# Kernel optimization log

Hardware: AMD Instinct MI355X
Metric: run time of the kernel (lower is better)

## Reference

```python
import jax, jax.numpy as jnp
import numpy as np

NB_HEAD = 8
SIZE_PER_HEAD = 64
EMB = 512  # word embedding dim; output_dim = NB_HEAD*SIZE_PER_HEAD = 512
B, S = 8, 4096


def setup_inputs() -> dict:
    key = jax.random.key(0)
    ks = jax.random.split(key, 8)
    return {
        "Q_seq": jax.random.normal(ks[0], (B, S, EMB), dtype=jnp.float32),
        "K_seq": jax.random.normal(ks[1], (B, S, EMB), dtype=jnp.float32),
        "V_seq": jax.random.normal(ks[2], (B, S, EMB), dtype=jnp.float32),
        "Q_len": jax.random.randint(ks[3], (B, 1), 0, S, dtype=jnp.int32),
        "V_len": jax.random.randint(ks[4], (B, 1), 0, SIZE_PER_HEAD, dtype=jnp.int32),
        "WQ": jax.random.normal(ks[5], (EMB, NB_HEAD * SIZE_PER_HEAD), dtype=jnp.float32),
        "WK": jax.random.normal(ks[6], (EMB, NB_HEAD * SIZE_PER_HEAD), dtype=jnp.float32),
        "WV": jax.random.normal(ks[7], (EMB, NB_HEAD * SIZE_PER_HEAD), dtype=jnp.float32),
    }


def _proj_heads(x, W):
    # [B,S,E] @ [E,H*d] -> [B,H,S,d]
    y = jnp.einsum('bse,eo->bso', x, W)
    y = y.reshape(y.shape[0], y.shape[1], NB_HEAD, SIZE_PER_HEAD)
    return jnp.transpose(y, (0, 2, 1, 3))


def reference(Q_seq, K_seq, V_seq, Q_len, V_len, WQ, WK, WV):
    H, d = NB_HEAD, SIZE_PER_HEAD
    Q = _proj_heads(Q_seq, WQ)  # [B,H,S,d]
    K = _proj_heads(K_seq, WK)
    V = _proj_heads(V_seq, WV)

    A = (Q * K) / jnp.asarray(d, Q.dtype) ** 0.5  # elementwise, [B,H,S,d]

    # TF code transposes A to [B,d,S,H] and masks along axis 1 (size d) using
    # V_len, then transposes back. Equivalent: additive mask on the LAST axis.
    vmask = jax.nn.one_hot(V_len[:, 0], d, dtype=A.dtype)       # [B,d]
    vmask = 1.0 - jnp.cumsum(vmask, axis=1)                      # [B,d]
    A = A - (1.0 - vmask)[:, None, None, :] * 1e12

    A = jax.nn.softmax(A, axis=-1)  # softmax over d (last axis), as tf.nn.softmax

    O = A * V                              # [B,H,S,d]
    O = jnp.transpose(O, (0, 2, 1, 3))     # [B,S,H,d]
    O = O.reshape(O.shape[0], O.shape[1], H * d)  # [B,S,H*d]

    # multiplicative mask over sequence axis using Q_len
    qmask = jax.nn.one_hot(Q_len[:, 0], O.shape[1], dtype=O.dtype)  # [B,S]
    qmask = 1.0 - jnp.cumsum(qmask, axis=1)
    return O * qmask[:, :, None]
```

## Files before the change

kernel.cpp:

```cpp
#include <hip/hip_runtime.h>

typedef unsigned short u16;
typedef _Float16 f16;
typedef _Float16 f16x4 __attribute__((ext_vector_type(4)));
typedef _Float16 f16x8 __attribute__((ext_vector_type(8)));
typedef float    f32x4 __attribute__((ext_vector_type(4)));

#define BATCH 8
#define SEQ   4096
#define EMB   512
#define NCOL  512

__global__ __launch_bounds__(256) void prep_w(
    const float* __restrict__ Wq, const float* __restrict__ Wk,
    const float* __restrict__ Wv, u16* __restrict__ out)
{
  __shared__ u16 tile[64][65];
  const int z = blockIdx.z;
  const float* in = (z < 2) ? Wq : (z < 4) ? Wk : Wv;
  const bool lo = (z == 1 || z == 3);
  u16* o = out + (size_t)z * EMB * NCOL;
  const int r0 = blockIdx.y * 64, c0 = blockIdx.x * 64;
  const int tx = threadIdx.x, ty = threadIdx.y;
#pragma unroll
  for (int i = 0; i < 16; ++i) {
    const int r = ty * 16 + i;
    const float x = in[(size_t)(r0 + r) * NCOL + (c0 + tx)];
    const f16 h = (f16)x;
    const f16 v = lo ? (f16)((x - (float)h) * 256.0f) : h;
    tile[r][tx] = __builtin_bit_cast(u16, v);
  }
  __syncthreads();
#pragma unroll
  for (int i = 0; i < 16; ++i) {
    const int rr = ty * 16 + i;
    o[(size_t)(c0 + rr) * EMB + (r0 + tx)] = tile[tx][rr];
  }
}

#define PSTRIDE 40
#define PLANE   (64*PSTRIDE)
#define BUFSZ   (5*PLANE)

__global__ __launch_bounds__(512, 2) void fused_attn(
    const float* __restrict__ Xq, const float* __restrict__ Xk,
    const float* __restrict__ Xv,
    const int* __restrict__ Qlen, const int* __restrict__ Vlen,
    const u16* __restrict__ Wt,
    float* __restrict__ out)
{
  const int b  = blockIdx.z;
  const int s0 = blockIdx.x * 64;
  const int c0 = blockIdx.y * 256;
  const int qlen = Qlen[b];
  const int t = threadIdx.x;

  if (s0 >= qlen) {
    const f32x4 z4 = {0.f, 0.f, 0.f, 0.f};
#pragma unroll
    for (int it = 0; it < 8; ++it) {
      const int f4  = it * 512 + t;
      const int row = f4 >> 6;
      const int col = (f4 & 63) * 4;
      *(f32x4*)(out + (size_t)(b * SEQ + s0 + row) * NCOL + c0 + col) = z4;
    }
    return;
  }
  const int vlen = Vlen[b];
  const int vl = (vlen == 0) ? 64 : vlen;

  __shared__ f16 smem[2 * BUFSZ] __attribute__((aligned(16)));

  const int w    = t >> 6;
  const int lane = t & 63;
  const int quad = lane >> 4;
  const int l15  = lane & 15;

  const int    srow = t >> 3;
  const int    sk4  = (t & 7) * 4;
  const size_t xg   = (size_t)(b * SEQ + s0 + srow) * EMB + sk4;
  const int    swo  = srow * PSTRIDE + sk4;

  const size_t wb = (size_t)(c0 + w * 32 + l15) * EMB + quad * 8;
  const u16* Wqh_g = Wt                + wb;
  const u16* Wql_g = Wt + 1 * EMB*NCOL + wb;
  const u16* Wkh_g = Wt + 2 * EMB*NCOL + wb;
  const u16* Wkl_g = Wt + 3 * EMB*NCOL + wb;
  const u16* Wv_g  = Wt + 4 * EMB*NCOL + wb;

  const int ao = l15 * PSTRIDE + quad * 8;

  f32x4 accQ[4][2], accQc[4][2], accK[4][2], accKc[4][2], accV[4][2];
#pragma unroll
  for (int rt = 0; rt < 4; ++rt)
#pragma unroll
    for (int ct = 0; ct < 2; ++ct) {
      const f32x4 z = {0.f, 0.f, 0.f, 0.f};
      accQ[rt][ct] = z; accQc[rt][ct] = z;
      accK[rt][ct] = z; accKc[rt][ct] = z;
      accV[rt][ct] = z;
    }

  f32x4 rq, rk, rv;

#define LOADX(TT) do { \
    rq = *(const f32x4*)(Xq + xg + (TT) * 32); \
    rk = *(const f32x4*)(Xk + xg + (TT) * 32); \
    rv = *(const f32x4*)(Xv + xg + (TT) * 32); \
  } while (0)

#define STAGE(BOFS) do { \
    f16* p_ = smem + (BOFS); \
    f16x4 qh_, ql_, kh_, kl_, vh_; \
    _Pragma("unroll") \
    for (int j = 0; j < 4; ++j) { \
      const float xq_ = rq[j]; const f16 qhh_ = (f16)xq_; \
      qh_[j] = qhh_; ql_[j] = (f16)((xq_ - (float)qhh_) * 256.0f); \
      const float xk_ = rk[j]; const f16 khh_ = (f16)xk_; \
      kh_[j] = khh_; kl_[j] = (f16)((xk_ - (float)khh_) * 256.0f); \
      vh_[j] = (f16)rv[j]; \
    } \
    *(f16x4*)(p_ + 0 * PLANE + swo) = qh_; \
    *(f16x4*)(p_ + 1 * PLANE + swo) = ql_; \
    *(f16x4*)(p_ + 2 * PLANE + swo) = kh_; \
    *(f16x4*)(p_ + 3 * PLANE + swo) = kl_; \
    *(f16x4*)(p_ + 4 * PLANE + swo) = vh_; \
  } while (0)

#define COMPUTE(BOFS, KK) do { \
    const f16* p_ = smem + (BOFS); \
    const int kk_ = (KK); \
    f16x8 bqh_[2], bql_[2], bkh_[2], bkl_[2], bv_[2]; \
    _Pragma("unroll") \
    for (int ct = 0; ct < 2; ++ct) { \
      const size_t wo_ = (size_t)ct * 16 * EMB + kk_; \
      bqh_[ct] = *(const f16x8*)(Wqh_g + wo_); \
      bql_[ct] = *(const f16x8*)(Wql_g + wo_); \
      bkh_[ct] = *(const f16x8*)(Wkh_g + wo_); \
      bkl_[ct] = *(const f16x8*)(Wkl_g + wo_); \
      bv_ [ct] = *(const f16x8*)(Wv_g  + wo_); \
    } \
    _Pragma("unroll") \
    for (int rt = 0; rt < 4; ++rt) { \
      const int ao_ = ao + rt * 16 * PSTRIDE; \
      const f16x8 aqh_ = *(const f16x8*)(p_ + 0 * PLANE + ao_); \
      const f16x8 aql_ = *(const f16x8*)(p_ + 1 * PLANE + ao_); \
      const f16x8 akh_ = *(const f16x8*)(p_ + 2 * PLANE + ao_); \
      const f16x8 akl_ = *(const f16x8*)(p_ + 3 * PLANE + ao_); \
      const f16x8 av_  = *(const f16x8*)(p_ + 4 * PLANE + ao_); \
      _Pragma("unroll") \
      for (int ct = 0; ct < 2; ++ct) { \
        accQ [rt][ct] = __builtin_amdgcn_mfma_f32_16x16x32_f16(aqh_, bqh_[ct], accQ [rt][ct], 0, 0, 0); \
        accQc[rt][ct] = __builtin_amdgcn_mfma_f32_16x16x32_f16(aqh_, bql_[ct], accQc[rt][ct], 0, 0, 0); \
        accQc[rt][ct] = __builtin_amdgcn_mfma_f32_16x16x32_f16(aql_, bqh_[ct], accQc[rt][ct], 0, 0, 0); \
        accK [rt][ct] = __builtin_amdgcn_mfma_f32_16x16x32_f16(akh_, bkh_[ct], accK [rt][ct], 0, 0, 0); \
        accKc[rt][ct] = __builtin_amdgcn_mfma_f32_16x16x32_f16(akh_, bkl_[ct], accKc[rt][ct], 0, 0, 0); \
        accKc[rt][ct] = __builtin_amdgcn_mfma_f32_16x16x32_f16(akl_, bkh_[ct], accKc[rt][ct], 0, 0, 0); \
        accV [rt][ct] = __builtin_amdgcn_mfma_f32_16x16x32_f16(av_,  bv_[ct],  accV [rt][ct], 0, 0, 0); \
      } \
    } \
  } while (0)

  LOADX(0);
  STAGE(0);
  __syncthreads();

#pragma unroll 1
  for (int tt = 0; tt < 16; tt += 2) {
    LOADX(tt + 1);
    COMPUTE(0, tt * 32);
    STAGE(BUFSZ);
    __syncthreads();
    if (tt < 14) LOADX(tt + 2);
    COMPUTE(BUFSZ, (tt + 1) * 32);
    if (tt < 14) STAGE(0);
    __syncthreads();
  }

#undef LOADX
#undef STAGE
#undef COMPUTE

  const float scale = 0.125f;
  const float rs    = 1.0f / 256.0f;
  float* smf = (float*)smem;

  float eA[4][2][4];
  float lm[4][4], lsum[4][4];

#pragma unroll
  for (int rt = 0; rt < 4; ++rt) {
#pragma unroll
    for (int r = 0; r < 4; ++r) {
      float a[2]; bool msk[2];
      float mx = -3.0e38f;
#pragma unroll
      for (int ct = 0; ct < 2; ++ct) {
        const float q = accQ[rt][ct][r] + accQc[rt][ct][r] * rs;
        const float k = accK[rt][ct][r] + accKc[rt][ct][r] * rs;
        a[ct] = q * k * scale;
        msk[ct] = ((w & 1) * 32 + ct * 16 + l15) < vl;
        if (msk[ct]) mx = fmaxf(mx, a[ct]);
      }
#pragma unroll
      for (int off = 1; off < 16; off <<= 1) mx = fmaxf(mx, __shfl_xor(mx, off));
      float sum = 0.f;
#pragma unroll
      for (int ct = 0; ct < 2; ++ct) {
        const float e = msk[ct] ? __expf(a[ct] - mx) : 0.0f;
        eA[rt][ct][r] = e;
        sum += e;
      }
#pragma unroll
      for (int off = 1; off < 16; off <<= 1) sum += __shfl_xor(sum, off);
      lm[rt][r] = mx; lsum[rt][r] = sum;
      const int row = rt * 16 + quad * 4 + r;
      if (l15 == 0) {
        smf[(w * 64 + row) * 2 + 0] = mx;
        smf[(w * 64 + row) * 2 + 1] = sum;
      }
    }
  }
  __syncthreads();

#pragma unroll
  for (int rt = 0; rt < 4; ++rt) {
#pragma unroll
    for (int r = 0; r < 4; ++r) {
      const int row = rt * 16 + quad * 4 + r;
      const int s   = s0 + row;
      const float pm = smf[((w ^ 1) * 64 + row) * 2 + 0];
      const float ps = smf[((w ^ 1) * 64 + row) * 2 + 1];
      const float m  = lm[rt][r];
      const float M  = fmaxf(m, pm);
      const float S  = lsum[rt][r] * __expf(m - M) + ps * __expf(pm - M);
      const float qm = (s < qlen) ? 1.0f : 0.0f;
      const float f  = __expf(m - M) * qm / S;
      const size_t ob = (size_t)(b * SEQ + s) * NCOL + c0 + w * 32 + l15;
      out[ob]      = eA[rt][0][r] * f * accV[rt][0][r];
      out[ob + 16] = eA[rt][1][r] * f * accV[rt][1][r];
    }
  }
}

extern "C" void kernel_launch(void* const* d_in, const int* in_sizes, int n_in,
                              void* d_out, int out_size, void* d_ws, size_t ws_size,
                              hipStream_t stream) {
  const float* Xq   = (const float*)d_in[0];
  const float* Xk   = (const float*)d_in[1];
  const float* Xv   = (const float*)d_in[2];
  const int*   Qlen = (const int*)d_in[3];
  const int*   Vlen = (const int*)d_in[4];
  const float* Wq   = (const float*)d_in[5];
  const float* Wk   = (const float*)d_in[6];
  const float* Wv   = (const float*)d_in[7];
  u16*   Wt  = (u16*)d_ws;
  float* out = (float*)d_out;

  dim3 pg(8, 8, 5), pb(64, 4, 1);
  prep_w<<<pg, pb, 0, stream>>>(Wq, Wk, Wv, Wt);

  dim3 g(SEQ / 64, NCOL / 256, BATCH), blk(512, 1, 1);
  fused_attn<<<g, blk, 0, stream>>>(Xq, Xk, Xv, Qlen, Vlen, Wt, out);
}
```

Measured before the change: 378.8 us.

## Fold split-f16 correction terms into main accumulators and swizzle LDS layout

The low-part scale factor drops from 256 to 16, and the high parts are pre-scaled by 1/16 in f16 so that the hi*lo cross products accumulate straight into the Q and K accumulators. This removes the separate correction accumulators and the final recombination, which frees accumulator registers. The padded LDS stride of 40 is replaced by a dense 32-wide row with an XOR swizzle to avoid bank conflicts while shrinking shared memory. Scaling the f16 operands by 1/16 adds extra VALU multiplies and may cost some precision, because the low parts carry fewer effective bits.

```diff
diff --git a/kernel.cpp b/kernel.cpp
--- a/kernel.cpp
+++ b/kernel.cpp
@@ -27,7 +27,7 @@
     const int r = ty * 16 + i;
     const float x = in[(size_t)(r0 + r) * NCOL + (c0 + tx)];
     const f16 h = (f16)x;
-    const f16 v = lo ? (f16)((x - (float)h) * 256.0f) : h;
+    const f16 v = lo ? (f16)((x - (float)h) * 16.0f) : h;
     tile[r][tx] = __builtin_bit_cast(u16, v);
   }
   __syncthreads();
@@ -38,9 +38,8 @@
   }
 }
 
-#define PSTRIDE 40
-#define PLANE   (64*PSTRIDE)
-#define BUFSZ   (5*PLANE)
+#define PLANE 2048
+#define BUFSZ (5*PLANE)
 
 __global__ __launch_bounds__(512, 2) void fused_attn(
     const float* __restrict__ Xq, const float* __restrict__ Xk,
@@ -77,9 +76,9 @@
   const int l15  = lane & 15;
 
   const int    srow = t >> 3;
-  const int    sk4  = (t & 7) * 4;
-  const size_t xg   = (size_t)(b * SEQ + s0 + srow) * EMB + sk4;
-  const int    swo  = srow * PSTRIDE + sk4;
+  const int    sj   = t & 7;
+  const size_t xg   = (size_t)(b * SEQ + s0 + srow) * EMB + sj * 4;
+  const int    swo  = srow * 32 + (((sj >> 1) ^ ((srow >> 1) & 3)) * 8) + (sj & 1) * 4;
 
   const size_t wb = (size_t)(c0 + w * 32 + l15) * EMB + quad * 8;
   const u16* Wqh_g = Wt                + wb;
@@ -88,17 +87,16 @@
   const u16* Wkl_g = Wt + 3 * EMB*NCOL + wb;
   const u16* Wv_g  = Wt + 4 * EMB*NCOL + wb;
 
-  const int ao = l15 * PSTRIDE + quad * 8;
-
-  f32x4 accQ[4][2], accQc[4][2], accK[4][2], accKc[4][2], accV[4][2];
+  const int swz = (l15 >> 1) & 3;
+  const int ao  = l15 * 32 + ((quad ^ swz) * 8);
+
+  f32x4 accQ[4][2], accK[4][2], accV[4][2];
 #pragma unroll
   for (int rt = 0; rt < 4; ++rt)
 #pragma unroll
     for (int ct = 0; ct < 2; ++ct) {
       const f32x4 z = {0.f, 0.f, 0.f, 0.f};
-      accQ[rt][ct] = z; accQc[rt][ct] = z;
-      accK[rt][ct] = z; accKc[rt][ct] = z;
-      accV[rt][ct] = z;
+      accQ[rt][ct] = z; accK[rt][ct] = z; accV[rt][ct] = z;
     }
 
   f32x4 rq, rk, rv;
@@ -115,9 +113,9 @@
     _Pragma("unroll") \
     for (int j = 0; j < 4; ++j) { \
       const float xq_ = rq[j]; const f16 qhh_ = (f16)xq_; \
-      qh_[j] = qhh_; ql_[j] = (f16)((xq_ - (float)qhh_) * 256.0f); \
+      qh_[j] = qhh_; ql_[j] = (f16)((xq_ - (float)qhh_) * 16.0f); \
       const float xk_ = rk[j]; const f16 khh_ = (f16)xk_; \
-      kh_[j] = khh_; kl_[j] = (f16)((xk_ - (float)khh_) * 256.0f); \
+      kh_[j] = khh_; kl_[j] = (f16)((xk_ - (float)khh_) * 16.0f); \
       vh_[j] = (f16)rv[j]; \
     } \
     *(f16x4*)(p_ + 0 * PLANE + swo) = qh_; \
@@ -130,6 +128,7 @@
 #define COMPUTE(BOFS, KK) do { \
     const f16* p_ = smem + (BOFS); \
     const int kk_ = (KK); \
+     \
     f16x8 bqh_[2], bql_[2], bkh_[2], bkl_[2], bv_[2]; \
     _Pragma("unroll") \
     for (int ct = 0; ct < 2; ++ct) { \
@@ -140,24 +139,60 @@
       bkl_[ct] = *(const f16x8*)(Wkl_g + wo_); \
       bv_ [ct] = *(const f16x8*)(Wv_g  + wo_); \
     } \
+     \
+    { \
+      f16x8 b4_[2]; \
+      _Pragma("unroll") \
+      for (int ct = 0; ct < 2; ++ct) \
+        _Pragma("unroll") \
+        for (int jj = 0; jj < 8; ++jj) b4_[ct][jj] = bqh_[ct][jj] * (f16)0.0625f; \
+      _Pragma("unroll") \
+      for (int rt = 0; rt < 4; ++rt) { \
+        const int ao_ = ao + rt * 512; \
+        const f16x8 ah_ = *(const f16x8*)(p_ + 0 * PLANE + ao_); \
+        const f16x8 al_ = *(const f16x8*)(p_ + 1 * PLANE + ao_); \
+        f16x8 a4_; \
+        _Pragma("unroll") \
+        for (int jj = 0; jj < 8; ++jj) a4_[jj] = ah_[jj] * (f16)0.0625f; \
+        _Pragma("unroll") \
+        for (int ct = 0; ct < 2; ++ct) { \
+          accQ[rt][ct] = __builtin_amdgcn_mfma_f32_16x16x32_f16(ah_, bqh_[ct], accQ[rt][ct], 0, 0, 0); \
+          accQ[rt][ct] = __builtin_amdgcn_mfma_f32_16x16x32_f16(a4_, bql_[ct], accQ[rt][ct], 0, 0, 0); \
+          accQ[rt][ct] = __builtin_amdgcn_mfma_f32_16x16x32_f16(al_, b4_[ct],  accQ[rt][ct], 0, 0, 0); \
+        } \
+      } \
+    } \
+     \
+    { \
+      f16x8 b4_[2]; \
+      _Pragma("unroll") \
+      for (int ct = 0; ct < 2; ++ct) \
+        _Pragma("unroll") \
+        for (int jj = 0; jj < 8; ++jj) b4_[ct][jj] = bkh_[ct][jj] * (f16)0.0625f; \
+      _Pragma("unroll") \
+      for (int rt = 0; rt < 4; ++rt) { \
+        const int ao_ = ao + rt * 512; \
+        const f16x8 ah_ = *(const f16x8*)(p_ + 2 * PLANE + ao_); \
+        const f16x8 al_ = *(const f16x8*)(p_ + 3 * PLANE + ao_); \
+        f16x8 a4_; \
+        _Pragma("unroll") \
+        for (int jj = 0; jj < 8; ++jj) a4_[jj] = ah_[jj] * (f16)0.0625f; \
+        _Pragma("unroll") \
+        for (int ct = 0; ct < 2; ++ct) { \
+          accK[rt][ct] = __builtin_amdgcn_mfma_f32_16x16x32_f16(ah_, bkh_[ct], accK[rt][ct], 0, 0, 0); \
+          accK[rt][ct] = __builtin_amdgcn_mfma_f32_16x16x32_f16(a4_, bkl_[ct], accK[rt][ct], 0, 0, 0); \
+          accK[rt][ct] = __builtin_amdgcn_mfma_f32_16x16x32_f16(al_, b4_[ct],  accK[rt][ct], 0, 0, 0); \
+        } \
+      } \
+    } \
+     \
     _Pragma("unroll") \
     for (int rt = 0; rt < 4; ++rt) { \
-      const int ao_ = ao + rt * 16 * PSTRIDE; \
-      const f16x8 aqh_ = *(const f16x8*)(p_ + 0 * PLANE + ao_); \
-      const f16x8 aql_ = *(const f16x8*)(p_ + 1 * PLANE + ao_); \
-      const f16x8 akh_ = *(const f16x8*)(p_ + 2 * PLANE + ao_); \
-      const f16x8 akl_ = *(const f16x8*)(p_ + 3 * PLANE + ao_); \
-      const f16x8 av_  = *(const f16x8*)(p_ + 4 * PLANE + ao_); \
-      _Pragma("unroll") \
-      for (int ct = 0; ct < 2; ++ct) { \
-        accQ [rt][ct] = __builtin_amdgcn_mfma_f32_16x16x32_f16(aqh_, bqh_[ct], accQ [rt][ct], 0, 0, 0); \
-        accQc[rt][ct] = __builtin_amdgcn_mfma_f32_16x16x32_f16(aqh_, bql_[ct], accQc[rt][ct], 0, 0, 0); \
-        accQc[rt][ct] = __builtin_amdgcn_mfma_f32_16x16x32_f16(aql_, bqh_[ct], accQc[rt][ct], 0, 0, 0); \
-        accK [rt][ct] = __builtin_amdgcn_mfma_f32_16x16x32_f16(akh_, bkh_[ct], accK [rt][ct], 0, 0, 0); \
-        accKc[rt][ct] = __builtin_amdgcn_mfma_f32_16x16x32_f16(akh_, bkl_[ct], accKc[rt][ct], 0, 0, 0); \
-        accKc[rt][ct] = __builtin_amdgcn_mfma_f32_16x16x32_f16(akl_, bkh_[ct], accKc[rt][ct], 0, 0, 0); \
-        accV [rt][ct] = __builtin_amdgcn_mfma_f32_16x16x32_f16(av_,  bv_[ct],  accV [rt][ct], 0, 0, 0); \
-      } \
+      const int ao_ = ao + rt * 512; \
+      const f16x8 av_ = *(const f16x8*)(p_ + 4 * PLANE + ao_); \
+      _Pragma("unroll") \
+      for (int ct = 0; ct < 2; ++ct) \
+        accV[rt][ct] = __builtin_amdgcn_mfma_f32_16x16x32_f16(av_, bv_[ct], accV[rt][ct], 0, 0, 0); \
     } \
   } while (0)
 
@@ -182,7 +217,6 @@
 #undef COMPUTE
 
   const float scale = 0.125f;
-  const float rs    = 1.0f / 256.0f;
   float* smf = (float*)smem;
 
   float eA[4][2][4];
@@ -196,8 +230,8 @@
       float mx = -3.0e38f;
 #pragma unroll
       for (int ct = 0; ct < 2; ++ct) {
-        const float q = accQ[rt][ct][r] + accQc[rt][ct][r] * rs;
-        const float k = accK[rt][ct][r] + accKc[rt][ct][r] * rs;
+        const float q = accQ[rt][ct][r];
+        const float k = accK[rt][ct][r];
         a[ct] = q * k * scale;
         msk[ct] = ((w & 1) * 32 + ct * 16 + l15) < vl;
         if (msk[ct]) mx = fmaxf(mx, a[ct]);
```

New measurement: 357.4 us. 5.7% less time.
